# Kernel optimization log

Hardware: AMD Instinct MI355X
Metric: run time of the kernel (lower is better)

The kernel has to match this reference:

```python
import jax, jax.numpy as jnp
import numpy as np

B, TV, F, H, V, NSTEPS = 64, 40, 2048, 1024, 32000, 30


def setup_inputs() -> dict:
    key = jax.random.key(0)
    ks = jax.random.split(key, 26)
    s = 0.02
    return {
        "batch_size": B,
        "action_feat": jax.random.normal(ks[0], (B, TV, F), jnp.float32),
        "imagenet_feat": jax.random.normal(ks[1], (B, TV, F), jnp.float32),
        "video_mask": jnp.ones((B, TV), jnp.float32),
        "captions": jax.random.randint(ks[2], (B, NSTEPS + 1), 0, V),
        "caption_mask": jnp.ones((B, NSTEPS + 1), jnp.float32),
        "enc_img_W": jax.random.normal(ks[3], (F, H), jnp.float32) * s,
        "enc_img_b": jax.random.normal(ks[4], (H,), jnp.float32) * s,
        "enc_mean_W": jax.random.normal(ks[5], (F, H), jnp.float32) * s,
        "enc_mean_b": jax.random.normal(ks[6], (H,), jnp.float32) * s,
        "att_w": jax.random.normal(ks[7], (H,), jnp.float32) * s,
        "att_Wa": jax.random.normal(ks[8], (H, H), jnp.float32) * s,
        "att_Ua": jax.random.normal(ks[9], (H, H), jnp.float32) * s,
        "att_ba": jax.random.normal(ks[10], (H,), jnp.float32) * s,
        "Wemb": jax.random.normal(ks[11], (V, H), jnp.float32) * s,
        "embed_word_W": jax.random.normal(ks[12], (H, V), jnp.float32) * s,
        "embed_word_b": jax.random.normal(ks[13], (V,), jnp.float32) * s,
        "lstm1_Wih": jax.random.normal(ks[14], (4 * H, 2 * H), jnp.float32) * s,
        "lstm1_Whh": jax.random.normal(ks[15], (4 * H, H), jnp.float32) * s,
        "lstm1_bih": jax.random.normal(ks[16], (4 * H,), jnp.float32) * s,
        "lstm1_bhh": jax.random.normal(ks[17], (4 * H,), jnp.float32) * s,
        "lstm2_Wih": jax.random.normal(ks[18], (4 * H, H), jnp.float32) * s,
        "lstm2_Whh": jax.random.normal(ks[19], (4 * H, H), jnp.float32) * s,
        "lstm2_bih": jax.random.normal(ks[20], (4 * H,), jnp.float32) * s,
        "lstm2_bhh": jax.random.normal(ks[21], (4 * H,), jnp.float32) * s,
    }


def _lstm_cell(x, h, c, Wih, Whh, bih, bhh):
    # PyTorch LSTMCell: gates in order (i, f, g, o)
    g = x @ Wih.T + bih + h @ Whh.T + bhh
    i, f, gg, o = jnp.split(g, 4, axis=-1)
    c_new = jax.nn.sigmoid(f) * c + jax.nn.sigmoid(i) * jnp.tanh(gg)
    h_new = jax.nn.sigmoid(o) * jnp.tanh(c_new)
    return h_new, c_new


def reference(batch_size, action_feat, imagenet_feat, video_mask, captions,
              caption_mask, enc_img_W, enc_img_b, enc_mean_W, enc_mean_b,
              att_w, att_Wa, att_Ua, att_ba, Wemb, embed_word_W, embed_word_b,
              lstm1_Wih, lstm1_Whh, lstm1_bih, lstm1_bhh,
              lstm2_Wih, lstm2_Whh, lstm2_bih, lstm2_bhh):
    bsz = action_feat.shape[0]
    # source code overwrites cat(action, imagenet) with action_feat alone
    video_feat = action_feat @ enc_img_W + enc_img_b          # [B, Tv, H]
    vid_emb = jnp.transpose(video_feat, (1, 0, 2))            # [Tv, B, H]
    feat_mean = jnp.mean(action_feat, axis=1)                 # [B, F]
    feat_mean = feat_mean @ enc_mean_W + enc_mean_b           # [B, H]

    image_part = jnp.einsum('tbh,hk->tbk', vid_emb, att_Ua) + att_ba  # [Tv,B,H]
    vm = video_mask.T                                         # [Tv, B]

    n = captions.shape[1] - 1
    emb_seq = jnp.transpose(Wemb[captions[:, :n]], (1, 0, 2))  # [n, B, H]
    tgts = captions[:, 1:n + 1].T                              # [n, B]
    masks = caption_mask[:, 1:n + 1].T                         # [n, B]

    zeros_h = jnp.zeros((bsz, vid_emb.shape[-1]), jnp.float32)

    def step(carry, xs):
        h1, c1, h2, c2, h_prev, loss = carry
        emb_t, tgt_t, mask_t = xs
        # Bahdanau attention with custom masked softmax
        e = jnp.tanh(h_prev @ att_Wa + image_part)             # [Tv, B, H]
        e = jnp.einsum('tbh,h->tb', e, att_w)                  # [Tv, B]
        e_max = jnp.max(e, axis=0)                             # [B]
        e_hat = vm * jnp.exp(e - e_max)                        # [Tv, B]
        denom = jnp.sum(e_hat, axis=0)
        denom = denom + (denom == 0.0).astype(jnp.float32) + 1e-9
        e_div = e_hat / denom                                  # [Tv, B]
        atten = jnp.einsum('tb,tbh->bh', e_div, vid_emb)       # [B, H]

        x1 = jnp.concatenate([emb_t, atten], axis=1)           # [B, 2H]
        h1, c1 = _lstm_cell(x1, h1, c1, lstm1_Wih, lstm1_Whh, lstm1_bih, lstm1_bhh)
        h2, c2 = _lstm_cell(h1, h2, c2, lstm2_Wih, lstm2_Whh, lstm2_bih, lstm2_bhh)

        logits = h2 @ embed_word_W + embed_word_b              # [B, V]
        logp = jax.nn.log_softmax(logits, axis=-1)
        ce_mean = -jnp.mean(jnp.take_along_axis(logp, tgt_t[:, None], axis=1)[:, 0])
        # original: scalar mean-CE broadcast over mask, summed, / batch_size
        loss = loss + ce_mean * jnp.sum(mask_t) / bsz
        return (h1, c1, h2, c2, h2, loss), None

    init = (feat_mean, zeros_h, zeros_h, zeros_h, feat_mean, jnp.float32(0.0))
    (h1, c1, h2, c2, h_prev, total_loss), _ = jax.lax.scan(
        step, init, (emb_seq, tgts, masks))
    return total_loss
```

## Files before the change

### kernel.cpp

```cpp
#include <hip/hip_runtime.h>
#include <stdint.h>

constexpr int kB   = 64;
constexpr int kTV  = 40;
constexpr int kF   = 2048;
constexpr int kH   = 1024;
constexpr int kV   = 32000;
constexpr int kNS  = 30;
constexpr int kCAP = 31;

typedef __attribute__((ext_vector_type(8))) short bf16x8;
typedef __attribute__((ext_vector_type(4))) float f32x4;
typedef unsigned short us;

__device__ __forceinline__ float sigm(float x) { return 1.f / (1.f + __expf(-x)); }
__device__ __forceinline__ float tanh_fast(float x) {
    float e = __expf(2.f * x);
    return 1.f - 2.f / (e + 1.f);
}
__device__ __forceinline__ us f2bf(float x) {
    unsigned u = __float_as_uint(x);
    return (us)((u + 0x7fffu + ((u >> 16) & 1u)) >> 16);
}
__device__ __forceinline__ float bf2f(us u) {
    return __uint_as_float((unsigned)u << 16);
}

__device__ __forceinline__ void gl16(const us* g, us* lds) {
    __builtin_amdgcn_global_load_lds(
        (const __attribute__((address_space(1))) unsigned int*)(g),
        (__attribute__((address_space(3))) unsigned int*)(lds), 16, 0, 0);
}

template <int N>
__device__ __forceinline__ void waitv() {
    asm volatile("s_waitcnt vmcnt(%0)" :: "n"(N) : "memory");
}
__device__ __forceinline__ void barrier_raw() {
    __builtin_amdgcn_s_barrier();
    asm volatile("" ::: "memory");
}

__device__ __forceinline__ void store_packedA(us* base, int row, int col, us v) {
    int kt = col >> 5, kc = col & 31, ms = row >> 4;
    int l = (row & 15) + (((kc >> 2) & 3) << 4);
    int j = (kc & 3) + ((kc >> 4) << 2);
    base[((((size_t)kt * 4 + ms) * 64 + l) << 3) + j] = v;
}

template <int NSPW, int KT>
__device__ __forceinline__ void mfma_kloop(
    const us* __restrict__ Ap, const us* __restrict__ Bp,
    us* Asm, us* Bsm, int w, int l, f32x4 acc[4][NSPW])
{
    constexpr int BSTEP = 2048 * NSPW;
    constexpr int LPT = 1 + NSPW;
    auto stage = [&](int t, int slot) {
        gl16(Ap + (size_t)t * 2048 + w * 512 + l * 8, Asm + slot * 2048 + w * 512);
#pragma unroll
        for (int i = 0; i < NSPW; ++i)
            gl16(Bp + (size_t)t * BSTEP + (w * NSPW + i) * 512 + l * 8,
                 Bsm + slot * BSTEP + (w * NSPW + i) * 512);
    };
    stage(0, 0); stage(1, 1); stage(2, 2);
#pragma unroll 1
    for (int t = 0; t < KT; ++t) {
        int slot = t % 3;
        int rem = KT - 1 - t;
        if (rem >= 2) waitv<2 * LPT>();
        else if (rem == 1) waitv<LPT>();
        else waitv<0>();
        barrier_raw();
        bf16x8 bfr[NSPW], afr[4];
#pragma unroll
        for (int i = 0; i < NSPW; ++i)
            bfr[i] = *(const bf16x8*)(Bsm + slot * BSTEP + ((w * NSPW + i) * 64 + l) * 8);
#pragma unroll
        for (int ms = 0; ms < 4; ++ms)
            afr[ms] = *(const bf16x8*)(Asm + slot * 2048 + (ms * 64 + l) * 8);
#pragma unroll
        for (int ms = 0; ms < 4; ++ms)
#pragma unroll
            for (int i = 0; i < NSPW; ++i)
                acc[ms][i] = __builtin_amdgcn_mfma_f32_16x16x32_bf16(
                    afr[ms], bfr[i], acc[ms][i], 0, 0, 0);
        __builtin_amdgcn_sched_barrier(0);
        barrier_raw();
        if (t + 3 < KT) stage(t + 3, slot);
    }
}

__global__ __launch_bounds__(256) void prep_mean(
    const float* __restrict__ af, float* __restrict__ fm,
    const float* __restrict__ bih1, const float* __restrict__ bhh1,
    const float* __restrict__ bih2, const float* __restrict__ bhh2,
    const float* __restrict__ capmask,
    float* __restrict__ bsum1, float* __restrict__ bsum2, float* __restrict__ msum)
{
    int tid = threadIdx.x;
    if (blockIdx.x < 64) {
        int b = blockIdx.x;
        const float* base = af + (size_t)b * kTV * kF;
        float a[8] = {};
        for (int t = 0; t < kTV; ++t) {
            const float* rp = base + (size_t)t * kF + tid * 8;
            float4 v0 = *(const float4*)rp;
            float4 v1 = *(const float4*)(rp + 4);
            a[0] += v0.x; a[1] += v0.y; a[2] += v0.z; a[3] += v0.w;
            a[4] += v1.x; a[5] += v1.y; a[6] += v1.z; a[7] += v1.w;
        }
        float* op = fm + (size_t)b * kF + tid * 8;
#pragma unroll
        for (int j = 0; j < 8; ++j) op[j] = a[j] * (1.f / kTV);
    } else {
        int g = (blockIdx.x - 64) * 256 + tid;
        if (g < 4096) bsum1[g] = bih1[g] + bhh1[g];
        else if (g < 8192) { int j = g - 4096; bsum2[j] = bih2[j] + bhh2[j]; }
        else if (g < 8192 + kNS) {
            int t = g - 8192;
            float s = 0.f;
            for (int b = 0; b < kB; ++b) s += capmask[b * kCAP + t + 1];
            msum[t] = s;
        }
    }
}

__global__ __launch_bounds__(256) void pack_rm(
    const float* __restrict__ p0, int ld0, int ksplit,
    const float* __restrict__ p1, int ld1,
    int NGRP, int GS, int HS, int KT,
    us* __restrict__ out)
{
    __shared__ us tile[16][136];
    int kb = blockIdx.x * 128;
    int grp = blockIdx.y;
    int row0 = (grp % NGRP) * GS + (grp / NGRP) * HS;
    int tid = threadIdx.x;
    int r = tid >> 5, c4 = (tid & 31) * 4;
#pragma unroll
    for (int pass = 0; pass < 2; ++pass) {
        int rr = r + pass * 8;
        int row = row0 + rr;
        int k = kb + c4;
        float4 v;
        if (k < ksplit) v = *(const float4*)(p0 + (size_t)row * ld0 + k);
        else            v = *(const float4*)(p1 + (size_t)row * ld1 + (k - ksplit));
        ushort4 o; o.x = f2bf(v.x); o.y = f2bf(v.y); o.z = f2bf(v.z); o.w = f2bf(v.w);
        *(ushort4*)&tile[rr][c4] = o;
    }
    __syncthreads();
    int ktl = tid >> 6, l = tid & 63, ul = l & 15, q = (l >> 4) & 3;
    __align__(16) us o2[8];
#pragma unroll
    for (int j = 0; j < 8; ++j) {
        int kc = (j & 3) + q * 4 + ((j >> 2) << 4);
        o2[j] = tile[ul][ktl * 32 + kc];
    }
    int kt = (kb >> 5) + ktl;
    size_t base = (((size_t)(grp / NGRP) * KT + kt) * NGRP + (grp % NGRP)) * 512;
    *(uint4*)(out + base + (size_t)l * 8) = *(const uint4*)o2;
}

__global__ __launch_bounds__(256) void pack_cm(const float* __restrict__ W,
                                               us* __restrict__ out)
{
    __shared__ us tile[32][136];
    int n0 = blockIdx.x * 128, k0 = blockIdx.y * 32;
    int tid = threadIdx.x;
    int r = tid >> 5, c4 = (tid & 31) * 4;
#pragma unroll
    for (int pass = 0; pass < 4; ++pass) {
        int rr = r + pass * 8;
        float4 v = *(const float4*)(W + (size_t)(k0 + rr) * kV + n0 + c4);
        ushort4 o; o.x = f2bf(v.x); o.y = f2bf(v.y); o.z = f2bf(v.z); o.w = f2bf(v.w);
        *(ushort4*)&tile[rr][c4] = o;
    }
    __syncthreads();
    int ns = tid >> 5, lp = (tid & 31) * 2;
    size_t base = (((size_t)blockIdx.x * 32 + blockIdx.y) * 8 + ns) * 512;
    __align__(16) us o2[16];
#pragma unroll
    for (int li = 0; li < 2; ++li) {
        int l = lp + li, ul = l & 15, q = (l >> 4) & 3;
#pragma unroll
        for (int j = 0; j < 8; ++j) {
            int kc = (j & 3) + q * 4 + ((j >> 2) << 4);
            o2[li * 8 + j] = tile[kc][ns * 16 + ul];
        }
    }
    *(uint4*)(out + base + lp * 8) = *(const uint4*)&o2[0];
    *(uint4*)(out + base + lp * 8 + 8) = *(const uint4*)&o2[8];
}

__global__ __launch_bounds__(256) void pack_sm4(
    const float* __restrict__ Wi, const float* __restrict__ Wm,
    const float* __restrict__ Wua, const float* __restrict__ Wa,
    us* __restrict__ oi, us* __restrict__ om,
    us* __restrict__ oua, us* __restrict__ oa)
{
    int bid = blockIdx.x;
    const float* W; us* out; int KT, rel;
    if (bid < 512)       { W = Wi;  out = oi;  KT = 64; rel = bid; }
    else if (bid < 1024) { W = Wm;  out = om;  KT = 64; rel = bid - 512; }
    else if (bid < 1280) { W = Wua; out = oua; KT = 32; rel = bid - 1024; }
    else                 { W = Wa;  out = oa;  KT = 32; rel = bid - 1280; }
    int bx = rel & 7, by = rel >> 3;
    __shared__ us tile[32][136];
    int n0 = bx * 128, k0 = by * 32;
    int tid = threadIdx.x;
    int r = tid >> 5, c4 = (tid & 31) * 4;
#pragma unroll
    for (int pass = 0; pass < 4; ++pass) {
        int rr = r + pass * 8;
        float4 v = *(const float4*)(W + (size_t)(k0 + rr) * 1024 + n0 + c4);
        ushort4 o; o.x = f2bf(v.x); o.y = f2bf(v.y); o.z = f2bf(v.z); o.w = f2bf(v.w);
        *(ushort4*)&tile[rr][c4] = o;
    }
    __syncthreads();
    int ns = tid >> 5, lp = (tid & 31) * 2;
    int nb64 = bx * 2 + (ns >> 2), ns4 = ns & 3;
    size_t base = (((size_t)nb64 * KT + by) * 4 + ns4) * 512;
    __align__(16) us o2[16];
#pragma unroll
    for (int li = 0; li < 2; ++li) {
        int l = lp + li, ul = l & 15, q = (l >> 4) & 3;
#pragma unroll
        for (int j = 0; j < 8; ++j) {
            int kc = (j & 3) + q * 4 + ((j >> 2) << 4);
            o2[li * 8 + j] = tile[kc][ns * 16 + ul];
        }
    }
    *(uint4*)(out + base + lp * 8) = *(const uint4*)&o2[0];
    *(uint4*)(out + base + lp * 8 + 8) = *(const uint4*)&o2[8];
}

__global__ __launch_bounds__(256) void pack_emb(
    const float* __restrict__ Wemb, const int* __restrict__ captions,
    us* __restrict__ embP)
{
    __shared__ us tile[16][136];
    int rel = blockIdx.x;
    int s = rel / 32, rem = rel % 32;
    int rg = rem & 3, kb8 = rem >> 2;
    int tid = threadIdx.x;
    int r = tid >> 5, c4 = (tid & 31) * 4;
#pragma unroll
    for (int pass = 0; pass < 2; ++pass) {
        int rr = r + pass * 8;
        int b = rg * 16 + rr;
        int word = captions[b * kCAP + s];
        float4 v = *(const float4*)(Wemb + (size_t)word * kH + kb8 * 128 + c4);
        ushort4 o; o.x = f2bf(v.x); o.y = f2bf(v.y); o.z = f2bf(v.z); o.w = f2bf(v.w);
        *(ushort4*)&tile[rr][c4] = o;
    }
    __syncthreads();
    int ktl = tid >> 6, l = tid & 63, ul = l & 15, q = (l >> 4) & 3;
    __align__(16) us o2[8];
#pragma unroll
    for (int j = 0; j < 8; ++j) {
        int kc = (j & 3) + q * 4 + ((j >> 2) << 4);
        o2[j] = tile[ul][ktl * 32 + kc];
    }
    int kt = kb8 * 4 + ktl;
    size_t base = (((size_t)s * 32 + kt) * 4 + rg) * 512;
    *(uint4*)(embP + base + (size_t)l * 8) = *(const uint4*)o2;
}

template <int KT>
__global__ __launch_bounds__(256) void enc_gemm(
    const us* __restrict__ Ap, const us* __restrict__ Bp,
    const float* __restrict__ bias, float* __restrict__ outF,
    us* __restrict__ outP)
{
    __shared__ us Asm[3][2048];
    __shared__ us Bsm[3][2048];
    int tid = threadIdx.x, w = tid >> 6, l = tid & 63;
    int nb = blockIdx.x, mb = blockIdx.y;
    f32x4 acc[4][1] = {};
    mfma_kloop<1, KT>(Ap + (size_t)mb * KT * 2048, Bp + (size_t)nb * KT * 2048,
                      &Asm[0][0], &Bsm[0][0], w, l, acc);
    int ul = l & 15, sg = l >> 4;
    int n = nb * 64 + w * 16 + ul;
    float bv = bias[n];
#pragma unroll
    for (int ms = 0; ms < 4; ++ms)
#pragma unroll
        for (int r = 0; r < 4; ++r) {
            int rl = ms * 16 + sg * 4 + r;
            int row = mb * 64 + rl;
            float v = acc[ms][0][r] + bv;
            outF[(size_t)row * kH + n] = v;
            if (outP) store_packedA(outP + (size_t)mb * 65536, rl, n, f2bf(v));
        }
}

__global__ __launch_bounds__(256) void p3_gemm(
    const us* __restrict__ Ap, const us* __restrict__ Bp,
    const float* __restrict__ bias, us* __restrict__ xcat1p,
    us* __restrict__ h2hist0)
{
    __shared__ us Asm[3][2048];
    __shared__ us Bsm[3][2048];
    int tid = threadIdx.x, w = tid >> 6, l = tid & 63;
    int nb = blockIdx.x;
    f32x4 acc[4][1] = {};
    mfma_kloop<1, 64>(Ap, Bp + (size_t)nb * 64 * 2048, &Asm[0][0], &Bsm[0][0], w, l, acc);
    int ul = l & 15, sg = l >> 4;
    int n = nb * 64 + w * 16 + ul;
    float bv = bias[n];
#pragma unroll
    for (int ms = 0; ms < 4; ++ms)
#pragma unroll
        for (int r = 0; r < 4; ++r) {
            int row = ms * 16 + sg * 4 + r;
            us hb = f2bf(acc[ms][0][r] + bv);
            store_packedA(xcat1p, row, 1024 + n, hb);
            store_packedA(h2hist0, row, n, hb);
        }
}

__global__ __launch_bounds__(256) void gemb_gemm(
    const us* __restrict__ embP, const us* __restrict__ W1p,
    us* __restrict__ Gemb)
{
    __shared__ us Asm[3][2048];
    __shared__ us Bsm[3][2048];
    int rel = blockIdx.x;
    int s = rel >> 6, nb = rel & 63;
    int tid = threadIdx.x, w = tid >> 6, l = tid & 63;
    f32x4 acc[4][1] = {};
    mfma_kloop<1, 32>(embP + (size_t)s * 65536, W1p + (size_t)nb * 96 * 2048,
                      &Asm[0][0], &Bsm[0][0], w, l, acc);
    int ul = l & 15, sg = l >> 4;
    int n = nb * 64 + w * 16 + ul;
#pragma unroll
    for (int ms = 0; ms < 4; ++ms)
#pragma unroll
        for (int r = 0; r < 4; ++r) {
            int row = ms * 16 + sg * 4 + r;
            Gemb[((size_t)s * 64 + row) * 4096 + n] = f2bf(acc[ms][0][r]);
        }
}

__global__ __launch_bounds__(512) void hwa_gemm(
    const us* __restrict__ h2p, const us* __restrict__ WaP,
    float* __restrict__ hw)
{
    __shared__ __align__(16) char smem[49152];
    float* rsum = (float*)smem;
    int tid = threadIdx.x, w = tid >> 6, l = tid & 63, nb = blockIdx.x;
    int h = w >> 2, w4 = w & 3;
    us* Asm = (us*)(smem + h * 24576);
    us* Bsm = Asm + 6144;
    f32x4 acc[4][1] = {};
    mfma_kloop<1, 16>(h2p + (size_t)h * 16 * 2048,
                      WaP + (size_t)nb * 32 * 2048 + (size_t)h * 16 * 2048,
                      Asm, Bsm, w4, l, acc);
    int ul = l & 15, sg = l >> 4;
    __syncthreads();
    if (h == 1) {
#pragma unroll
        for (int ms = 0; ms < 4; ++ms)
#pragma unroll
            for (int r = 0; r < 4; ++r)
                rsum[((w4 * 64) + ms * 16 + sg * 4 + r) * 17 + ul] = acc[ms][0][r];
    }
    __syncthreads();
    if (h == 0) {
        int n = nb * 64 + w4 * 16 + ul;
#pragma unroll
        for (int ms = 0; ms < 4; ++ms)
#pragma unroll
            for (int r = 0; r < 4; ++r) {
                int row = ms * 16 + sg * 4 + r;
                hw[(size_t)row * kH + n] =
                    acc[ms][0][r] + rsum[((w4 * 64) + row) * 17 + ul];
            }
    }
}

__global__ __launch_bounds__(256) void attn_fused(
    const float* __restrict__ hw, const float* __restrict__ imgp,
    const float* __restrict__ attw, const float* __restrict__ vf,
    const float* __restrict__ vmask, us* __restrict__ xcat1p)
{
    __shared__ float hwv[kH];
    __shared__ float es[48];
    int b = blockIdx.x, tid = threadIdx.x;
    for (int i = tid; i < kH; i += 256) hwv[i] = hw[(size_t)b * kH + i];
    __syncthreads();
    int w = tid >> 6, l = tid & 63;
    for (int t = w; t < kTV; t += 4) {
        const float* ip = imgp + ((size_t)b * kTV + t) * kH;
        float p = 0.f;
#pragma unroll
        for (int hh = 0; hh < 16; ++hh) {
            int h = hh * 64 + l;
            p += tanh_fast(hwv[h] + ip[h]) * attw[h];
        }
        for (int off = 32; off; off >>= 1) p += __shfl_down(p, off);
        if (l == 0) es[t] = p;
    }
    __syncthreads();
    float mx = -1e30f;
    for (int t = 0; t < kTV; ++t) mx = fmaxf(mx, es[t]);
    const float* vm = vmask + b * kTV;
    float den = 0.f;
    for (int t = 0; t < kTV; ++t) den += vm[t] * __expf(es[t] - mx);
    den = den + (den == 0.f ? 1.f : 0.f) + 1e-9f;
    int h0 = tid * 4;
    float4 av = {0.f, 0.f, 0.f, 0.f};
    for (int t = 0; t < kTV; ++t) {
        float wgt = vm[t] * __expf(es[t] - mx) / den;
        float4 v = *(const float4*)(vf + ((size_t)b * kTV + t) * kH + h0);
        av.x += wgt * v.x; av.y += wgt * v.y; av.z += wgt * v.z; av.w += wgt * v.w;
    }
    store_packedA(xcat1p, b, h0 + 0, f2bf(av.x));
    store_packedA(xcat1p, b, h0 + 1, f2bf(av.y));
    store_packedA(xcat1p, b, h0 + 2, f2bf(av.z));
    store_packedA(xcat1p, b, h0 + 3, f2bf(av.w));
}

template <int KT, int BSTR, int KOFF>
__global__ __launch_bounds__(1024) void gates_cell(
    const us* __restrict__ Ap, const us* __restrict__ Bp,
    const float* __restrict__ bsum, const us* __restrict__ gemb,
    float* __restrict__ cbuf,
    us* __restrict__ dA, int ofsA, us* __restrict__ dB, int ofsB)
{
    __shared__ __align__(16) char smem[98304];
    float* gsm = (float*)smem;
    constexpr int KQ = KT / 4;
    int tid = threadIdx.x, w16 = tid >> 6, l = tid & 63, nb = blockIdx.x;
    int g = w16 >> 2, w4 = w16 & 3;
    us* Asm = (us*)(smem + g * 24576);
    us* Bsm = Asm + 6144;
    f32x4 acc[4][1] = {};
    mfma_kloop<1, KQ>(Ap + (size_t)g * KQ * 2048,
                      Bp + (size_t)nb * BSTR * 2048 + (size_t)(KOFF + g * KQ) * 2048,
                      Asm, Bsm, w4, l, acc);
    int ul = l & 15, sg = l >> 4;
    int sl = (g & 1) * 4 + w4;
    float bv = (g == 0) ? bsum[w4 * 1024 + nb * 16 + ul] : 0.f;
    __syncthreads();
    if (g < 2) {
#pragma unroll
        for (int ms = 0; ms < 4; ++ms)
#pragma unroll
            for (int r = 0; r < 4; ++r)
                gsm[(sl * 64 + ms * 16 + sg * 4 + r) * 17 + ul] = acc[ms][0][r] + bv;
    }
    __syncthreads();
    if (g >= 2) {
#pragma unroll
        for (int ms = 0; ms < 4; ++ms)
#pragma unroll
            for (int r = 0; r < 4; ++r)
                gsm[(sl * 64 + ms * 16 + sg * 4 + r) * 17 + ul] += acc[ms][0][r];
    }
    __syncthreads();
    {
        int row = tid >> 4, uc = tid & 15, u = nb * 16 + uc;
        float ge0 = 0.f, ge1 = 0.f, ge2 = 0.f, ge3 = 0.f;
        if (gemb) {
            const us* gp = gemb + (size_t)row * 4096 + nb * 64 + uc;
            ge0 = bf2f(gp[0]); ge1 = bf2f(gp[16]);
            ge2 = bf2f(gp[32]); ge3 = bf2f(gp[48]);
        }
        float gi = gsm[((0 * 64) + row) * 17 + uc] + gsm[((4 * 64) + row) * 17 + uc] + ge0;
        float gf = gsm[((1 * 64) + row) * 17 + uc] + gsm[((5 * 64) + row) * 17 + uc] + ge1;
        float gg = gsm[((2 * 64) + row) * 17 + uc] + gsm[((6 * 64) + row) * 17 + uc] + ge2;
        float go = gsm[((3 * 64) + row) * 17 + uc] + gsm[((7 * 64) + row) * 17 + uc] + ge3;
        float c = sigm(gf) * cbuf[(size_t)row * kH + u] + sigm(gi) * tanh_fast(gg);
        cbuf[(size_t)row * kH + u] = c;
        us hb = f2bf(sigm(go) * tanh_fast(c));
        store_packedA(dA, row, ofsA + u, hb);
        store_packedA(dB, row, ofsB + u, hb);
    }
}

__global__ __launch_bounds__(256) void logits_sb(
    const us* __restrict__ h2hist, const us* __restrict__ WvP,
    const float* __restrict__ embb, const int* __restrict__ captions,
    float* __restrict__ psumP, float* __restrict__ tlogs)
{
    constexpr int SBLK = 3;
    __shared__ us Asm[SBLK][3][2048];
    __shared__ us Bsm[3][4096];
    __shared__ float rsum[4][64];
    __shared__ int stgt[SBLK][64];
    int bid = blockIdx.x;
    int c = bid & 7, q = bid >> 3;
    int sgrp = q % 10, nb = c + (q / 10) * 8;
    if (nb >= 250) return;
    int s0 = sgrp * SBLK;
    int tid = threadIdx.x, w = tid >> 6, l = tid & 63, ul = l & 15, lsg = l >> 4;
    if (tid < 64)
#pragma unroll
        for (int si = 0; si < SBLK; ++si)
            stgt[si][tid] = captions[tid * kCAP + s0 + si + 1];
    const us* Ab0 = h2hist + (size_t)(s0 + 1) * 65536;
    const us* Ab1 = h2hist + (size_t)(s0 + 2) * 65536;
    const us* Ab2 = h2hist + (size_t)(s0 + 3) * 65536;
    const us* Bb  = WvP + (size_t)nb * 32 * 4096;
    auto stage = [&](int t, int slot) {
        gl16(Ab0 + (size_t)t * 2048 + w * 512 + l * 8, &Asm[0][slot][w * 512]);
        gl16(Ab1 + (size_t)t * 2048 + w * 512 + l * 8, &Asm[1][slot][w * 512]);
        gl16(Ab2 + (size_t)t * 2048 + w * 512 + l * 8, &Asm[2][slot][w * 512]);
#pragma unroll
        for (int i = 0; i < 2; ++i)
            gl16(Bb + (size_t)t * 4096 + (w * 2 + i) * 512 + l * 8,
                 &Bsm[slot][(w * 2 + i) * 512]);
    };
    f32x4 acc[SBLK][4][2] = {};
    stage(0, 0); stage(1, 1); stage(2, 2);
#pragma unroll 1
    for (int t = 0; t < 32; ++t) {
        int slot = t % 3;
        int rem = 31 - t;
        if (rem >= 2) waitv<10>();
        else if (rem == 1) waitv<5>();
        else waitv<0>();
        barrier_raw();
        bf16x8 b0 = *(const bf16x8*)&Bsm[slot][((w * 2 + 0) * 64 + l) * 8];
        bf16x8 b1 = *(const bf16x8*)&Bsm[slot][((w * 2 + 1) * 64 + l) * 8];
#pragma unroll
        for (int ms = 0; ms < 4; ++ms)
#pragma unroll
            for (int si = 0; si < SBLK; ++si) {
                bf16x8 a = *(const bf16x8*)&Asm[si][slot][(ms * 64 + l) * 8];
                acc[si][ms][0] = __builtin_amdgcn_mfma_f32_16x16x32_bf16(a, b0, acc[si][ms][0], 0, 0, 0);
                acc[si][ms][1] = __builtin_amdgcn_mfma_f32_16x16x32_bf16(a, b1, acc[si][ms][1], 0, 0, 0);
            }
        __builtin_amdgcn_sched_barrier(0);
        barrier_raw();
        if (t + 3 < 32) stage(t + 3, slot);
    }
    int n0 = nb * 128 + (2 * w + 0) * 16 + ul;
    int n1 = nb * 128 + (2 * w + 1) * 16 + ul;
    float e0 = embb[n0], e1 = embb[n1];
#pragma unroll
    for (int si = 0; si < SBLK; ++si) {
        float ls[4][4];
#pragma unroll
        for (int ms = 0; ms < 4; ++ms)
#pragma unroll
            for (int r = 0; r < 4; ++r) {
                int row = ms * 16 + lsg * 4 + r;
                float v0 = acc[si][ms][0][r] + e0, v1 = acc[si][ms][1][r] + e1;
                ls[ms][r] = __expf(v0) + __expf(v1);
                if (n0 == stgt[si][row]) tlogs[(s0 + si) * 64 + row] = v0;
                if (n1 == stgt[si][row]) tlogs[(s0 + si) * 64 + row] = v1;
            }
#pragma unroll
        for (int m = 1; m < 16; m <<= 1)
#pragma unroll
            for (int ms = 0; ms < 4; ++ms)
#pragma unroll
                for (int r = 0; r < 4; ++r)
                    ls[ms][r] += __shfl_xor(ls[ms][r], m);
        if (ul == 0)
#pragma unroll
            for (int ms = 0; ms < 4; ++ms)
#pragma unroll
                for (int r = 0; r < 4; ++r)
                    rsum[w][ms * 16 + lsg * 4 + r] = ls[ms][r];
        __syncthreads();
        if (tid < 64)
            psumP[((size_t)(s0 + si) * 250 + nb) * 64 + tid] =
                rsum[0][tid] + rsum[1][tid] + rsum[2][tid] + rsum[3][tid];
        __syncthreads();
    }
}

__global__ __launch_bounds__(256) void final_loss(
    const float* __restrict__ psumP, const float* __restrict__ tlogs,
    const float* __restrict__ msum, float* __restrict__ out)
{
    __shared__ float sl[16000];
    int s = blockIdx.x, tid = threadIdx.x;
    const float* src = psumP + (size_t)s * 16000;
    for (int i = tid; i < 16000; i += 256) sl[i] = src[i];
    __syncthreads();
    if (tid < 64) {
        float tot = 0.f;
        for (int i = 0; i < 250; ++i) tot += sl[i * 64 + tid];
        float logp = tlogs[s * 64 + tid] - __logf(tot);
        float term = -logp * msum[s] * (1.f / 4096.f);
        for (int off = 32; off; off >>= 1) term += __shfl_down(term, off);
        if (tid == 0) atomicAdd(out, term);
    }
}

extern "C" void kernel_launch(void* const* d_in, const int* in_sizes, int n_in,
                              void* d_out, int out_size, void* d_ws, size_t ws_size,
                              hipStream_t stream)
{
    const float* action_feat = (const float*)d_in[1];
    const float* video_mask  = (const float*)d_in[3];
    const int*   captions    = (const int*)d_in[4];
    const float* capmask     = (const float*)d_in[5];
    const float* enc_img_W   = (const float*)d_in[6];
    const float* enc_img_b   = (const float*)d_in[7];
    const float* enc_mean_W  = (const float*)d_in[8];
    const float* enc_mean_b  = (const float*)d_in[9];
    const float* att_w       = (const float*)d_in[10];
    const float* att_Wa      = (const float*)d_in[11];
    const float* att_Ua      = (const float*)d_in[12];
    const float* att_ba      = (const float*)d_in[13];
    const float* Wemb        = (const float*)d_in[14];
    const float* embW        = (const float*)d_in[15];
    const float* embb        = (const float*)d_in[16];
    const float* W1ih        = (const float*)d_in[17];
    const float* W1hh        = (const float*)d_in[18];
    const float* b1ih        = (const float*)d_in[19];
    const float* b1hh        = (const float*)d_in[20];
    const float* W2ih        = (const float*)d_in[21];
    const float* W2hh        = (const float*)d_in[22];
    const float* b2ih        = (const float*)d_in[23];
    const float* b2hh        = (const float*)d_in[24];

    char* base = (char*)d_ws;
    size_t off = 0;
    auto alloc = [&](size_t bytes) {
        char* p = base + off;
        off = (off + bytes + 255) & ~(size_t)255;
        return p;
    };
    constexpr int BIG = 0x40000000;

    float* vf    = (float*)alloc((size_t)2560 * 1024 * 4);
    float* imgp  = (float*)alloc((size_t)2560 * 1024 * 4);
    float* fm    = (float*)alloc((size_t)64 * 2048 * 4);
    float* hw    = (float*)alloc((size_t)64 * 1024 * 4);
    float* bsum1 = (float*)alloc(4096 * 4);
    float* bsum2 = (float*)alloc(4096 * 4);
    float* msum  = (float*)alloc(32 * 4);
    float* psumP = (float*)alloc((size_t)kNS * 250 * 64 * 4);
    float* tlogs = (float*)alloc((size_t)kNS * 64 * 4);
    us* Gemb     = (us*)alloc((size_t)kNS * 64 * 4096 * 2);
    us* x2p0 = (us*)alloc((size_t)64 * 2048 * 2);
    us* x2p1 = (us*)alloc((size_t)64 * 2048 * 2);
    float* c1    = (float*)alloc((size_t)64 * 1024 * 4);
    float* c2    = (float*)alloc((size_t)64 * 1024 * 4);
    size_t zlen  = (size_t)((char*)(c2 + 64 * 1024) - (char*)x2p0);

    us* x1p0 = (us*)alloc((size_t)64 * 2048 * 2);
    us* x1p1 = (us*)alloc((size_t)64 * 2048 * 2);
    us* h2hist = (us*)alloc((size_t)(kNS + 1) * 64 * 1024 * 2);
    us* embP = (us*)alloc((size_t)kNS * 64 * 1024 * 2);
    us* afP  = (us*)alloc((size_t)2560 * 2048 * 2);
    us* vfP  = (us*)alloc((size_t)2560 * 1024 * 2);
    us* fmP  = (us*)alloc((size_t)64 * 2048 * 2);
    us* WiP  = (us*)alloc((size_t)2048 * 1024 * 2);
    us* WmP  = (us*)alloc((size_t)2048 * 1024 * 2);
    us* WuaP = (us*)alloc((size_t)1024 * 1024 * 2);
    us* WaP  = (us*)alloc((size_t)1024 * 1024 * 2);
    us* W1p  = (us*)alloc((size_t)3072 * 4096 * 2);
    us* W2p  = (us*)alloc((size_t)2048 * 4096 * 2);
    us* WvP  = (us*)alloc((size_t)1024 * 32000 * 2);
    if (off > ws_size) return;

    hipMemsetAsync(d_out, 0, 4, stream);
    hipMemsetAsync(x2p0, 0, zlen, stream);

    prep_mean<<<97, 256, 0, stream>>>(action_feat, fm, b1ih, b1hh, b2ih, b2hh,
                                      capmask, bsum1, bsum2, msum);
    pack_rm<<<dim3(16, 4), 256, 0, stream>>>(fm, 2048, BIG, nullptr, 0,
                                             4, 16, 64, 64, fmP);
    pack_rm<<<dim3(16, 160), 256, 0, stream>>>(action_feat, 2048, BIG, nullptr, 0,
                                               4, 16, 64, 64, afP);
    pack_rm<<<dim3(24, 256), 256, 0, stream>>>(W1ih, 2048, 2048, W1hh, 1024,
                                               4, 1024, 16, 96, W1p);
    pack_rm<<<dim3(16, 256), 256, 0, stream>>>(W2ih, 1024, 1024, W2hh, 1024,
                                               4, 1024, 16, 64, W2p);
    pack_sm4<<<1536, 256, 0, stream>>>(enc_img_W, enc_mean_W, att_Ua, att_Wa,
                                       WiP, WmP, WuaP, WaP);
    pack_cm<<<dim3(250, 32), 256, 0, stream>>>(embW, WvP);
    pack_emb<<<960, 256, 0, stream>>>(Wemb, captions, embP);

    enc_gemm<64><<<dim3(16, 40), 256, 0, stream>>>(afP, WiP, enc_img_b, vf, vfP);
    p3_gemm<<<16, 256, 0, stream>>>(fmP, WmP, enc_mean_b, x1p0, h2hist);
    enc_gemm<32><<<dim3(16, 40), 256, 0, stream>>>(vfP, WuaP, att_ba, imgp, nullptr);
    gemb_gemm<<<1920, 256, 0, stream>>>(embP, W1p, Gemb);

    for (int s = 0; s < kNS; ++s) {
        us* x1c = (s & 1) ? x1p1 : x1p0;
        us* x1n = (s & 1) ? x1p0 : x1p1;
        us* x2c = (s & 1) ? x2p1 : x2p0;
        us* x2n = (s & 1) ? x2p0 : x2p1;
        hwa_gemm<<<16, 512, 0, stream>>>(h2hist + (size_t)s * 65536, WaP, hw);
        attn_fused<<<64, 256, 0, stream>>>(hw, imgp, att_w, vf, video_mask, x1c);
        gates_cell<64, 96, 32><<<64, 1024, 0, stream>>>(
            x1c, W1p, bsum1, Gemb + (size_t)s * 64 * 4096, c1,
            x1n, 1024, x2c, 0);
        gates_cell<64, 64, 0><<<64, 1024, 0, stream>>>(
            x2c, W2p, bsum2, nullptr, c2,
            x2n, 1024, h2hist + (size_t)(s + 1) * 65536, 0);
    }
    logits_sb<<<2560, 256, 0, stream>>>(h2hist, WvP, embb, captions, psumP, tlogs);
    final_loss<<<kNS, 256, 0, stream>>>(psumP, tlogs, msum, (float*)d_out);
}
```

Baseline: 2.000 ms.

## Fuse attention Wa projection into LSTM2 gate kernel via split-K partial sums

The per-step hwa_gemm launch is removed. The LSTM2 cell kernel now multiplies each block's freshly computed 16-unit h2 slice by a matching slice of a specially packed Wa, and writes 64 partial [64x1024] products that attn_fused sums on load. This drops one kernel launch and one serial dependency per timestep, but adds extra global traffic for the partial sums (16MB written and read per step) and zero-padded MFMA work. Separately, logits_sb goes from triple to double buffering, cutting LDS use at some cost in latency hiding.

```diff
diff --git a/kernel.cpp b/kernel.cpp
--- a/kernel.cpp
+++ b/kernel.cpp
@@ -234,6 +234,25 @@
     *(uint4*)(out + base + lp * 8 + 8) = *(const uint4*)&o2[8];
 }
 
+__global__ __launch_bounds__(256) void pack_wae(const float* __restrict__ Wa,
+                                                us* __restrict__ WaE)
+{
+    int nb = blockIdx.x >> 4, cb = blockIdx.x & 15;
+    int tid = threadIdx.x;
+    int ns = tid >> 6, l = tid & 63;
+    int ul = l & 15, q = (l >> 4) & 3;
+    int col = cb * 64 + ns * 16 + ul;
+    __align__(16) us o[8];
+#pragma unroll
+    for (int j = 0; j < 4; ++j) {
+        int k = (j & 3) + q * 4;
+        o[j] = f2bf(Wa[(size_t)(nb * 16 + k) * kH + col]);
+    }
+    o[4] = 0; o[5] = 0; o[6] = 0; o[7] = 0;
+    size_t base = (((size_t)(nb * 16 + cb)) * 4 + ns) * 512;
+    *(uint4*)(WaE + base + (size_t)l * 8) = *(const uint4*)o;
+}
+
 __global__ __launch_bounds__(256) void pack_emb(
     const float* __restrict__ Wemb, const int* __restrict__ captions,
     us* __restrict__ embP)
@@ -380,14 +399,25 @@
 }
 
 __global__ __launch_bounds__(256) void attn_fused(
-    const float* __restrict__ hw, const float* __restrict__ imgp,
-    const float* __restrict__ attw, const float* __restrict__ vf,
-    const float* __restrict__ vmask, us* __restrict__ xcat1p)
+    const float* __restrict__ hw0, const float* __restrict__ hwP,
+    const float* __restrict__ imgp, const float* __restrict__ attw,
+    const float* __restrict__ vf, const float* __restrict__ vmask,
+    us* __restrict__ xcat1p)
 {
     __shared__ float hwv[kH];
     __shared__ float es[48];
     int b = blockIdx.x, tid = threadIdx.x;
-    for (int i = tid; i < kH; i += 256) hwv[i] = hw[(size_t)b * kH + i];
+    if (hw0) {
+        for (int i = tid; i < kH; i += 256) hwv[i] = hw0[(size_t)b * kH + i];
+    } else {
+        int c4 = tid * 4;
+        float4 a = {0.f, 0.f, 0.f, 0.f};
+        for (int nb = 0; nb < 64; ++nb) {
+            float4 v = *(const float4*)(hwP + ((size_t)nb * 64 + b) * 1024 + c4);
+            a.x += v.x; a.y += v.y; a.z += v.z; a.w += v.w;
+        }
+        *(float4*)&hwv[c4] = a;
+    }
     __syncthreads();
     int w = tid >> 6, l = tid & 63;
     for (int t = w; t < kTV; t += 4) {
@@ -479,14 +509,98 @@
     }
 }
 
+__global__ __launch_bounds__(1024) void gates2_cell(
+    const us* __restrict__ Ap, const us* __restrict__ Bp,
+    const float* __restrict__ bsum, float* __restrict__ cbuf,
+    us* __restrict__ dA, int ofsA, us* __restrict__ dB, int ofsB,
+    float* __restrict__ hwPart, const us* __restrict__ WaE)
+{
+    __shared__ __align__(16) char smem[98304];
+    float* gsm = (float*)smem;
+    us* hA = (us*)(smem + 40960);
+    constexpr int KQ = 16;
+    int tid = threadIdx.x, w16 = tid >> 6, l = tid & 63, nb = blockIdx.x;
+    int g = w16 >> 2, w4 = w16 & 3;
+    us* Asm = (us*)(smem + g * 24576);
+    us* Bsm = Asm + 6144;
+    f32x4 acc[4][1] = {};
+    mfma_kloop<1, KQ>(Ap + (size_t)g * KQ * 2048,
+                      Bp + (size_t)nb * 64 * 2048 + (size_t)(g * KQ) * 2048,
+                      Asm, Bsm, w4, l, acc);
+    int ul = l & 15, sg = l >> 4;
+    int sl = (g & 1) * 4 + w4;
+    float bv = (g == 0) ? bsum[w4 * 1024 + nb * 16 + ul] : 0.f;
+    __syncthreads();
+    if (g < 2) {
+#pragma unroll
+        for (int ms = 0; ms < 4; ++ms)
+#pragma unroll
+            for (int r = 0; r < 4; ++r)
+                gsm[(sl * 64 + ms * 16 + sg * 4 + r) * 17 + ul] = acc[ms][0][r] + bv;
+    }
+    __syncthreads();
+    if (g >= 2) {
+#pragma unroll
+        for (int ms = 0; ms < 4; ++ms)
+#pragma unroll
+            for (int r = 0; r < 4; ++r)
+                gsm[(sl * 64 + ms * 16 + sg * 4 + r) * 17 + ul] += acc[ms][0][r];
+    }
+    __syncthreads();
+    int row = tid >> 4, uc = tid & 15, u = nb * 16 + uc;
+    {
+        float gi = gsm[((0 * 64) + row) * 17 + uc] + gsm[((4 * 64) + row) * 17 + uc];
+        float gf = gsm[((1 * 64) + row) * 17 + uc] + gsm[((5 * 64) + row) * 17 + uc];
+        float gg = gsm[((2 * 64) + row) * 17 + uc] + gsm[((6 * 64) + row) * 17 + uc];
+        float go = gsm[((3 * 64) + row) * 17 + uc] + gsm[((7 * 64) + row) * 17 + uc];
+        float c = sigm(gf) * cbuf[(size_t)row * kH + u] + sigm(gi) * tanh_fast(gg);
+        cbuf[(size_t)row * kH + u] = c;
+        us hb = f2bf(sigm(go) * tanh_fast(c));
+        store_packedA(dA, row, ofsA + u, hb);
+        store_packedA(dB, row, ofsB + u, hb);
+        if (hwPart) {
+            *(unsigned*)(hA + tid * 2) = 0;
+            __syncthreads();
+            int lpos = (row & 15) + (((uc >> 2) & 3) << 4);
+            hA[((((row >> 4) * 64) + lpos) << 3) + (uc & 3)] = hb;
+            __syncthreads();
+            int cb = w16;
+            f32x4 hacc[4][4] = {};
+            bf16x8 afr[4];
+#pragma unroll
+            for (int ms = 0; ms < 4; ++ms)
+                afr[ms] = *(const bf16x8*)(hA + (ms * 64 + l) * 8);
+#pragma unroll
+            for (int ns = 0; ns < 4; ++ns) {
+                bf16x8 bfr = *(const bf16x8*)(WaE +
+                    ((((size_t)(nb * 16 + cb)) * 4 + ns) << 9) + l * 8);
+#pragma unroll
+                for (int ms = 0; ms < 4; ++ms)
+                    hacc[ms][ns] = __builtin_amdgcn_mfma_f32_16x16x32_bf16(
+                        afr[ms], bfr, hacc[ms][ns], 0, 0, 0);
+            }
+#pragma unroll
+            for (int ms = 0; ms < 4; ++ms)
+#pragma unroll
+                for (int ns = 0; ns < 4; ++ns)
+#pragma unroll
+                    for (int r = 0; r < 4; ++r) {
+                        int row2 = ms * 16 + sg * 4 + r;
+                        int col = cb * 64 + ns * 16 + ul;
+                        hwPart[((size_t)nb * 64 + row2) * 1024 + col] = hacc[ms][ns][r];
+                    }
+        }
+    }
+}
+
 __global__ __launch_bounds__(256) void logits_sb(
     const us* __restrict__ h2hist, const us* __restrict__ WvP,
     const float* __restrict__ embb, const int* __restrict__ captions,
     float* __restrict__ psumP, float* __restrict__ tlogs)
 {
     constexpr int SBLK = 3;
-    __shared__ us Asm[SBLK][3][2048];
-    __shared__ us Bsm[3][4096];
+    __shared__ us Asm[SBLK][2][2048];
+    __shared__ us Bsm[2][4096];
     __shared__ float rsum[4][64];
     __shared__ int stgt[SBLK][64];
     int bid = blockIdx.x;
@@ -513,13 +627,11 @@
                  &Bsm[slot][(w * 2 + i) * 512]);
     };
     f32x4 acc[SBLK][4][2] = {};
-    stage(0, 0); stage(1, 1); stage(2, 2);
+    stage(0, 0); stage(1, 1);
 #pragma unroll 1
     for (int t = 0; t < 32; ++t) {
-        int slot = t % 3;
-        int rem = 31 - t;
-        if (rem >= 2) waitv<10>();
-        else if (rem == 1) waitv<5>();
+        int slot = t & 1;
+        if (t < 31) waitv<5>();
         else waitv<0>();
         barrier_raw();
         bf16x8 b0 = *(const bf16x8*)&Bsm[slot][((w * 2 + 0) * 64 + l) * 8];
@@ -534,7 +646,7 @@
             }
         __builtin_amdgcn_sched_barrier(0);
         barrier_raw();
-        if (t + 3 < 32) stage(t + 3, slot);
+        if (t + 2 < 32) stage(t + 2, slot);
     }
     int n0 = nb * 128 + (2 * w + 0) * 16 + ul;
     int n1 = nb * 128 + (2 * w + 1) * 16 + ul;
@@ -633,6 +745,7 @@
     float* imgp  = (float*)alloc((size_t)2560 * 1024 * 4);
     float* fm    = (float*)alloc((size_t)64 * 2048 * 4);
     float* hw    = (float*)alloc((size_t)64 * 1024 * 4);
+    float* hwPart= (float*)alloc((size_t)64 * 64 * 1024 * 4);
     float* bsum1 = (float*)alloc(4096 * 4);
     float* bsum2 = (float*)alloc(4096 * 4);
     float* msum  = (float*)alloc(32 * 4);
@@ -656,6 +769,7 @@
     us* WmP  = (us*)alloc((size_t)2048 * 1024 * 2);
     us* WuaP = (us*)alloc((size_t)1024 * 1024 * 2);
     us* WaP  = (us*)alloc((size_t)1024 * 1024 * 2);
+    us* WaE  = (us*)alloc((size_t)64 * 16 * 4 * 512 * 2);
     us* W1p  = (us*)alloc((size_t)3072 * 4096 * 2);
     us* W2p  = (us*)alloc((size_t)2048 * 4096 * 2);
     us* WvP  = (us*)alloc((size_t)1024 * 32000 * 2);
@@ -676,6 +790,7 @@
                                                4, 1024, 16, 64, W2p);
     pack_sm4<<<1536, 256, 0, stream>>>(enc_img_W, enc_mean_W, att_Ua, att_Wa,
                                        WiP, WmP, WuaP, WaP);
+    pack_wae<<<1024, 256, 0, stream>>>(att_Wa, WaE);
     pack_cm<<<dim3(250, 32), 256, 0, stream>>>(embW, WvP);
     pack_emb<<<960, 256, 0, stream>>>(Wemb, captions, embP);
 
@@ -683,20 +798,22 @@
     p3_gemm<<<16, 256, 0, stream>>>(fmP, WmP, enc_mean_b, x1p0, h2hist);
     enc_gemm<32><<<dim3(16, 40), 256, 0, stream>>>(vfP, WuaP, att_ba, imgp, nullptr);
     gemb_gemm<<<1920, 256, 0, stream>>>(embP, W1p, Gemb);
+    hwa_gemm<<<16, 512, 0, stream>>>(h2hist, WaP, hw);
 
     for (int s = 0; s < kNS; ++s) {
         us* x1c = (s & 1) ? x1p1 : x1p0;
         us* x1n = (s & 1) ? x1p0 : x1p1;
         us* x2c = (s & 1) ? x2p1 : x2p0;
         us* x2n = (s & 1) ? x2p0 : x2p1;
-        hwa_gemm<<<16, 512, 0, stream>>>(h2hist + (size_t)s * 65536, WaP, hw);
-        attn_fused<<<64, 256, 0, stream>>>(hw, imgp, att_w, vf, video_mask, x1c);
+        attn_fused<<<64, 256, 0, stream>>>(
+            (s == 0) ? hw : nullptr, hwPart, imgp, att_w, vf, video_mask, x1c);
         gates_cell<64, 96, 32><<<64, 1024, 0, stream>>>(
             x1c, W1p, bsum1, Gemb + (size_t)s * 64 * 4096, c1,
             x1n, 1024, x2c, 0);
-        gates_cell<64, 64, 0><<<64, 1024, 0, stream>>>(
-            x2c, W2p, bsum2, nullptr, c2,
-            x2n, 1024, h2hist + (size_t)(s + 1) * 65536, 0);
+        gates2_cell<<<64, 1024, 0, stream>>>(
+            x2c, W2p, bsum2, c2,
+            x2n, 1024, h2hist + (size_t)(s + 1) * 65536, 0,
+            (s < kNS - 1) ? hwPart : nullptr, WaE);
     }
     logits_sb<<<2560, 256, 0, stream>>>(h2hist, WvP, embb, captions, psumP, tlogs);
     final_loss<<<kNS, 256, 0, stream>>>(psumP, tlogs, msum, (float*)d_out);
```

Measured after the change: 2.042 ms. 2.1% more time.
